# Optimization experiments

Hardware: AMD Instinct MI355X
Metric: run time of the kernel (lower is better)

The kernel has to match this reference:

```python
import jax, jax.numpy as jnp
import numpy as np
from jax import lax

B, D, BOND, OUT = 16384, 784, 5, 10

def setup_inputs() -> dict:
    key = jax.random.key(0)
    k = jax.random.split(key, 6)
    x = jax.random.uniform(k[0], (B, D), dtype=jnp.float32)
    core_first = jax.random.normal(k[1], (1, 2, BOND), dtype=jnp.float32) * 0.1
    cores_mid = jax.random.normal(k[2], (D - 2, BOND, 2, BOND), dtype=jnp.float32) * 0.1
    core_last = jax.random.normal(k[3], (BOND, 2, 1), dtype=jnp.float32) * 0.1
    # xavier_uniform for fc.weight with fan_in=1, fan_out=OUT
    bound = float(np.sqrt(6.0 / (1 + OUT)))
    fc_w = jax.random.uniform(k[4], (OUT, 1), dtype=jnp.float32, minval=-bound, maxval=bound)
    fc_b = jnp.zeros((OUT,), dtype=jnp.float32)
    return {"x": x, "core_first": core_first, "cores_mid": cores_mid,
            "core_last": core_last, "fc_w": fc_w, "fc_b": fc_b}

def reference(x, core_first, cores_mid, core_last, fc_w, fc_b):
    # x: [B, D] -> feature map [B, D, 2] = stack(1-x, x)
    xs = jnp.stack([1.0 - x, x], axis=-1)            # [B, D, 2]
    # first core: (1, 2, bond) -> initial carry [B, bond]
    carry0 = jnp.einsum('bi,ir->br', xs[:, 0], core_first[0])  # [B, bond]
    # sequential tensor-train contraction over middle sites via scan
    xs_mid = jnp.moveaxis(xs[:, 1:-1], 1, 0)          # [D-2, B, 2]
    def step(carry, inp):
        xi, core = inp                                # xi: [B,2], core: [bond,2,bond]
        carry = jnp.einsum('bl,bi,lir->br', carry, xi, core)
        return carry, None
    carry, _ = lax.scan(step, carry0, (xs_mid, cores_mid))
    # last core: (bond, 2, 1) -> scalar per batch element
    vlast = jnp.einsum('bi,li->bl', xs[:, -1], core_last[:, :, 0])  # [B, bond]
    res = jnp.sum(carry * vlast, axis=-1, keepdims=True)            # [B, 1]
    out = res @ fc_w.T + fc_b                          # [B, OUT]
    return out
```

## Files before the change

### kernel.cpp

```cpp
#include <hip/hip_runtime.h>


typedef float v4f __attribute__((ext_vector_type(4)));
typedef float v2f __attribute__((ext_vector_type(2)));

constexpr int Bn     = 16384;
constexpr int Dn     = 784;
constexpr int NOUT   = 10;
constexpr int NPAIR  = 390;
constexpr int PVEC   = 41;
constexpr int PMAT   = 22;
constexpr int RHP0   = 195;
constexpr int BWD_P0 = 349;
constexpr int PAIR_F = 100;
constexpr int PAIR_V = 25;

__device__ __forceinline__ v4f splat4(float x) { v4f v = {x, x, x, x}; return v; }
__device__ __forceinline__ v4f fma4(v4f a, v4f b, v4f c) {
    return __builtin_elementwise_fma(a, b, c);
}

struct Frag { v4f r[5]; float c4[5]; };
struct CMat { v4f row[5]; v4f c4v; float c44; };

__device__ __forceinline__ void build_C2(const float* s, v2f xA, v2f xB,
                                         CMat& CA, CMat& CB) {
    const float aA = xA[0], bA = xA[1], pA = aA * bA;
    const float aB = xB[0], bB = xB[1], pB = aB * bB;
    const v4f vaA = splat4(aA), vbA = splat4(bA), vpA = splat4(pA);
    const v4f vaB = splat4(aB), vbB = splat4(bB), vpB = splat4(pB);
    const v4f* s4 = (const v4f*)s;
#pragma unroll
    for (int l = 0; l < 5; ++l) {
        v4f q0 = s4[l], q1 = s4[5 + l], q2 = s4[10 + l], q3 = s4[15 + l];
        CA.row[l] = fma4(vpA, q3, fma4(vbA, q2, fma4(vaA, q1, q0)));
        CB.row[l] = fma4(vpB, q3, fma4(vbB, q2, fma4(vaB, q1, q0)));
    }
    {
        v4f q0 = s4[20], q1 = s4[21], q2 = s4[22], q3 = s4[23];
        CA.c4v = fma4(vpA, q3, fma4(vbA, q2, fma4(vaA, q1, q0)));
        CB.c4v = fma4(vpB, q3, fma4(vbB, q2, fma4(vaB, q1, q0)));
    }
    {
        v4f q = s4[24];
        CA.c44 = fmaf(pA, q[3], fmaf(bA, q[2], fmaf(aA, q[1], q[0])));
        CB.c44 = fmaf(pB, q[3], fmaf(bB, q[2], fmaf(aB, q[1], q[0])));
    }
}

__device__ __forceinline__ void matmul(const Frag& M, const CMat& C, Frag& T) {
#pragma unroll
    for (int i = 0; i < 5; ++i) {
        v4f acc  = splat4(M.r[i][0]) * C.row[0];
        float a4 = M.r[i][0] * C.c4v[0];
#pragma unroll
        for (int l = 1; l < 4; ++l) {
            acc = fma4(splat4(M.r[i][l]), C.row[l], acc);
            a4  = fmaf(M.r[i][l], C.c4v[l], a4);
        }
        acc = fma4(splat4(M.c4[i]), C.row[4], acc);
        a4  = fmaf(M.c4[i], C.c44, a4);
        T.r[i] = acc; T.c4[i] = a4;
    }
}

__device__ __forceinline__ void vecstep(v4f& cv, float& c4, const CMat& C) {
    v4f acc  = splat4(cv[0]) * C.row[0];
    float a4 = cv[0] * C.c4v[0];
#pragma unroll
    for (int l = 1; l < 4; ++l) {
        acc = fma4(splat4(cv[l]), C.row[l], acc);
        a4  = fmaf(cv[l], C.c4v[l], a4);
    }
    acc = fma4(splat4(c4), C.row[4], acc);
    a4  = fmaf(c4, C.c44, a4);
    cv = acc; c4 = a4;
}

__device__ __forceinline__ void sload(const v4f* src, v4f& a, v4f& b, int lane) {
    a = src[lane];
    if (lane < 36) b = src[64 + lane];
}
__device__ __forceinline__ void swrite(v4f* dst, v4f a, v4f b, int lane) {
    dst[lane] = a;
    if (lane < 36) dst[64 + lane] = b;
}

__global__ void prepack_pairs(const float* __restrict__ cm, float* __restrict__ pk)
{
    int idx = blockIdx.x * 256 + threadIdx.x;
    if (idx >= NPAIR * 100) return;
    int p = idx / 100, rest = idx - p * 100;
    int q = rest / 25, e = rest - q * 25;
    int l = e / 5, r = e - l * 5;
    int m1 = 2 * p + 1, m2 = 2 * p + 2;
    const float* L = cm + (size_t)(m1 * 5 + l) * 10;
    float acc = 0.f;
#pragma unroll
    for (int k = 0; k < 5; ++k) {
        float Lk = (q & 1) ? (L[5 + k] - L[k]) : L[k];
        const float* R = cm + (size_t)(m2 * 5 + k) * 10;
        float Rk = (q & 2) ? (R[5 + r] - R[r]) : R[r];
        acc = fmaf(Lk, Rk, acc);
    }
    int wl = l, wr = r;
    if (p >= BWD_P0) { wl = r; wr = l; }
    int off;
    if (wr < 4)      off = q * 20 + wl * 4 + wr;
    else if (wl < 4) off = 80 + q * 4 + wl;
    else             off = 96 + q;
    pk[(size_t)p * PAIR_F + off] = acc;
}

__global__ __launch_bounds__(512, 2)
void mps_half_kernel(const float* __restrict__ x,
                     const float* __restrict__ core_first,
                     const float* __restrict__ cores_mid,
                     const float* __restrict__ core_last,
                     const float* __restrict__ pk,
                     float* __restrict__ out)
{
    __shared__ v4f   pkbuf[8][2][100];
    __shared__ float matbuf[7][25][128];

    const int lane = threadIdx.x & 63;
    const int wave = threadIdx.x >> 6;
    const int g    = blockIdx.x >> 1;
    const int h    = blockIdx.x & 1;
    const int rowA = g * 128 + lane;
    const int rowB = rowA + 64;
    const v2f* __restrict__ xA2 = (const v2f*)(x + (size_t)rowA * Dn);
    const v2f* __restrict__ xB2 = (const v2f*)(x + (size_t)rowB * Dn);
    const v4f* __restrict__ pk4 = (const v4f*)pk;

    v4f* buf0 = &pkbuf[wave][0][0];
    v4f* buf1 = &pkbuf[wave][1][0];

    const bool isvec = (h == 0) ? (wave == 0) : (wave == 7);

    if (!isvec) {
        const int slot = (h == 0) ? (wave - 1) : wave;
        const int p0   = (h == 0) ? (PVEC + PMAT * (wave - 1))
                                  : (RHP0 + PMAT * wave);
        v4f sa, sb;
        sload(pk4 + (size_t)p0 * PAIR_V, sa, sb, lane);
        swrite(buf0, sa, sb, lane);
        sload(pk4 + (size_t)(p0 + 4) * PAIR_V, sa, sb, lane);
        v2f cA0 = xA2[p0 + 1], cA1 = xA2[p0 + 2], cA2 = xA2[p0 + 3], cA3 = xA2[p0 + 4];
        v2f cB0 = xB2[p0 + 1], cB1 = xB2[p0 + 2], cB2 = xB2[p0 + 3], cB3 = xB2[p0 + 4];

        Frag MA, TA, MB, TB;
        MA.r[0] = {1,0,0,0}; MA.r[1] = {0,1,0,0}; MA.r[2] = {0,0,1,0};
        MA.r[3] = {0,0,0,1}; MA.r[4] = {0,0,0,0};
        MA.c4[0] = 0; MA.c4[1] = 0; MA.c4[2] = 0; MA.c4[3] = 0; MA.c4[4] = 1;
        MB = MA;

#pragma unroll 1
        for (int c = 0; c < 6; ++c) {
            v4f* wb = (c & 1) ? buf0 : buf1;
            const float* rb = (const float*)((c & 1) ? buf1 : buf0);
            swrite(wb, sa, sb, lane);
            int ns = p0 + 4 * (c + 2);
            if (ns > NPAIR - 4) ns = NPAIR - 4;
            sload(pk4 + (size_t)ns * PAIR_V, sa, sb, lane);
            const int pn = p0 + 4 * (c + 1);
            v2f nA0 = xA2[pn + 1], nA1 = xA2[pn + 2], nA2 = xA2[pn + 3], nA3 = xA2[pn + 4];
            v2f nB0 = xB2[pn + 1], nB1 = xB2[pn + 2], nB2 = xB2[pn + 3], nB3 = xB2[pn + 4];
            CMat CA, CB;
            build_C2(rb + 0 * PAIR_F, cA0, cB0, CA, CB);
            matmul(MA, CA, TA); matmul(MB, CB, TB);
            build_C2(rb + 1 * PAIR_F, cA1, cB1, CA, CB);
            matmul(TA, CA, MA); matmul(TB, CB, MB);
            if (c < 5) {
                build_C2(rb + 2 * PAIR_F, cA2, cB2, CA, CB);
                matmul(MA, CA, TA); matmul(MB, CB, TB);
                build_C2(rb + 3 * PAIR_F, cA3, cB3, CA, CB);
                matmul(TA, CA, MA); matmul(TB, CB, MB);
            }
            cA0 = nA0; cA1 = nA1; cA2 = nA2; cA3 = nA3;
            cB0 = nB0; cB1 = nB1; cB2 = nB2; cB3 = nB3;
        }

#pragma unroll
        for (int i = 0; i < 5; ++i) {
#pragma unroll
            for (int r = 0; r < 4; ++r) {
                matbuf[slot][i * 5 + r][lane]      = MA.r[i][r];
                matbuf[slot][i * 5 + r][lane + 64] = MB.r[i][r];
            }
            matbuf[slot][i * 5 + 4][lane]      = MA.c4[i];
            matbuf[slot][i * 5 + 4][lane + 64] = MB.c4[i];
        }
        __syncthreads();
    } else if (h == 0) {
        v2f xA01 = xA2[0], xB01 = xB2[0];
        float clA[5], clB[5], cnA[5], cnB[5];
#pragma unroll
        for (int r = 0; r < 5; ++r) {
            float d = core_first[5 + r] - core_first[r];
            clA[r] = fmaf(xA01[0], d, core_first[r]);
            clB[r] = fmaf(xB01[0], d, core_first[r]);
        }
        const float* cm0 = cores_mid;
#pragma unroll
        for (int r = 0; r < 5; ++r) {
            float aA = 0.f, aB = 0.f;
#pragma unroll
            for (int l = 0; l < 5; ++l) {
                float base = cm0[l * 10 + r], d = cm0[l * 10 + 5 + r] - base;
                aA = fmaf(clA[l], fmaf(xA01[1], d, base), aA);
                aB = fmaf(clB[l], fmaf(xB01[1], d, base), aB);
            }
            cnA[r] = aA; cnB[r] = aB;
        }
        v4f cvA = {cnA[0], cnA[1], cnA[2], cnA[3]};
        v4f cvB = {cnB[0], cnB[1], cnB[2], cnB[3]};
        float c4A = cnA[4], c4B = cnB[4];

        v4f sa, sb;
        sload(pk4 + 0, sa, sb, lane);
        swrite(buf0, sa, sb, lane);
        sload(pk4 + (size_t)4 * PAIR_V, sa, sb, lane);
        v2f cA0 = xA2[1], cA1 = xA2[2], cA2 = xA2[3], cA3 = xA2[4];
        v2f cB0 = xB2[1], cB1 = xB2[2], cB2 = xB2[3], cB3 = xB2[4];

#pragma unroll 1
        for (int c = 0; c < 11; ++c) {
            v4f* wb = (c & 1) ? buf0 : buf1;
            const float* rb = (const float*)((c & 1) ? buf1 : buf0);
            swrite(wb, sa, sb, lane);
            int ns = 4 * (c + 2);
            if (ns > NPAIR - 4) ns = NPAIR - 4;
            sload(pk4 + (size_t)ns * PAIR_V, sa, sb, lane);
            const int pn = 4 * (c + 1);
            v2f nA0 = xA2[pn + 1], nA1 = xA2[pn + 2], nA2 = xA2[pn + 3], nA3 = xA2[pn + 4];
            v2f nB0 = xB2[pn + 1], nB1 = xB2[pn + 2], nB2 = xB2[pn + 3], nB3 = xB2[pn + 4];
            CMat CA, CB;
            build_C2(rb + 0 * PAIR_F, cA0, cB0, CA, CB);
            vecstep(cvA, c4A, CA); vecstep(cvB, c4B, CB);
            if (c < 10) {
                build_C2(rb + 1 * PAIR_F, cA1, cB1, CA, CB);
                vecstep(cvA, c4A, CA); vecstep(cvB, c4B, CB);
                build_C2(rb + 2 * PAIR_F, cA2, cB2, CA, CB);
                vecstep(cvA, c4A, CA); vecstep(cvB, c4B, CB);
                build_C2(rb + 3 * PAIR_F, cA3, cB3, CA, CB);
                vecstep(cvA, c4A, CA); vecstep(cvB, c4B, CB);
            }
            cA0 = nA0; cA1 = nA1; cA2 = nA2; cA3 = nA3;
            cB0 = nB0; cB1 = nB1; cB2 = nB2; cB3 = nB3;
        }
        clA[0] = cvA[0]; clA[1] = cvA[1]; clA[2] = cvA[2]; clA[3] = cvA[3]; clA[4] = c4A;
        clB[0] = cvB[0]; clB[1] = cvB[1]; clB[2] = cvB[2]; clB[3] = cvB[3]; clB[4] = c4B;

        __syncthreads();
#pragma unroll 1
        for (int w2 = 0; w2 < 7; ++w2) {
            float vA[5], vB[5];
#pragma unroll
            for (int r = 0; r < 5; ++r) {
                vA[r] = clA[0] * matbuf[w2][r][lane];
                vB[r] = clB[0] * matbuf[w2][r][lane + 64];
            }
#pragma unroll
            for (int l = 1; l < 5; ++l)
#pragma unroll
                for (int r = 0; r < 5; ++r) {
                    vA[r] = fmaf(clA[l], matbuf[w2][l * 5 + r][lane],      vA[r]);
                    vB[r] = fmaf(clB[l], matbuf[w2][l * 5 + r][lane + 64], vB[r]);
                }
#pragma unroll
            for (int r = 0; r < 5; ++r) { clA[r] = vA[r]; clB[r] = vB[r]; }
        }
        float* oA = out + (size_t)rowA * NOUT;
        float* oB = out + (size_t)rowB * NOUT;
#pragma unroll
        for (int i = 0; i < 5; ++i) { oA[i] = clA[i]; oB[i] = clB[i]; }
    } else {
        v2f xAz = xA2[391], xBz = xB2[391];
        float vlA[5], vlB[5], vnA[5], vnB[5];
#pragma unroll
        for (int l = 0; l < 5; ++l) {
            float base = core_last[2 * l], d = core_last[2 * l + 1] - base;
            vlA[l] = fmaf(xAz[1], d, base);
            vlB[l] = fmaf(xBz[1], d, base);
        }
        const float* cmL = cores_mid + (size_t)781 * 50;
#pragma unroll
        for (int l = 0; l < 5; ++l) {
            float aA = 0.f, aB = 0.f;
#pragma unroll
            for (int r = 0; r < 5; ++r) {
                float base = cmL[l * 10 + r], d = cmL[l * 10 + 5 + r] - base;
                aA = fmaf(fmaf(xAz[0], d, base), vlA[r], aA);
                aB = fmaf(fmaf(xBz[0], d, base), vlB[r], aB);
            }
            vnA[l] = aA; vnB[l] = aB;
        }
        v4f cvA = {vnA[0], vnA[1], vnA[2], vnA[3]};
        v4f cvB = {vnB[0], vnB[1], vnB[2], vnB[3]};
        float c4A = vnA[4], c4B = vnB[4];

        v4f sa, sb;
        sload(pk4 + (size_t)386 * PAIR_V, sa, sb, lane);
        swrite(buf0, sa, sb, lane);
        sload(pk4 + (size_t)382 * PAIR_V, sa, sb, lane);
        v2f cA0 = xA2[390], cA1 = xA2[389], cA2 = xA2[388], cA3 = xA2[387];
        v2f cB0 = xB2[390], cB1 = xB2[389], cB2 = xB2[388], cB3 = xB2[387];

#pragma unroll 1
        for (int c = 0; c < 11; ++c) {
            v4f* wb = (c & 1) ? buf0 : buf1;
            const float* rb = (const float*)((c & 1) ? buf1 : buf0);
            swrite(wb, sa, sb, lane);
            int ns = 386 - 4 * (c + 2);
            sload(pk4 + (size_t)ns * PAIR_V, sa, sb, lane);
            const int bn = 386 - 4 * (c + 1);
            v2f nA0 = xA2[bn + 4], nA1 = xA2[bn + 3], nA2 = xA2[bn + 2], nA3 = xA2[bn + 1];
            v2f nB0 = xB2[bn + 4], nB1 = xB2[bn + 3], nB2 = xB2[bn + 2], nB3 = xB2[bn + 1];
            CMat CA, CB;
            build_C2(rb + 3 * PAIR_F, cA0, cB0, CA, CB);
            vecstep(cvA, c4A, CA); vecstep(cvB, c4B, CB);
            if (c < 10) {
                build_C2(rb + 2 * PAIR_F, cA1, cB1, CA, CB);
                vecstep(cvA, c4A, CA); vecstep(cvB, c4B, CB);
                build_C2(rb + 1 * PAIR_F, cA2, cB2, CA, CB);
                vecstep(cvA, c4A, CA); vecstep(cvB, c4B, CB);
                build_C2(rb + 0 * PAIR_F, cA3, cB3, CA, CB);
                vecstep(cvA, c4A, CA); vecstep(cvB, c4B, CB);
            }
            cA0 = nA0; cA1 = nA1; cA2 = nA2; cA3 = nA3;
            cB0 = nB0; cB1 = nB1; cB2 = nB2; cB3 = nB3;
        }
        float uA[5] = {cvA[0], cvA[1], cvA[2], cvA[3], c4A};
        float uB[5] = {cvB[0], cvB[1], cvB[2], cvB[3], c4B};

        __syncthreads();
#pragma unroll 1
        for (int w2 = 6; w2 >= 0; --w2) {
            float vA[5], vB[5];
#pragma unroll
            for (int i = 0; i < 5; ++i) {
                float aA = matbuf[w2][i * 5][lane]      * uA[0];
                float aB = matbuf[w2][i * 5][lane + 64] * uB[0];
#pragma unroll
                for (int l = 1; l < 5; ++l) {
                    aA = fmaf(matbuf[w2][i * 5 + l][lane],      uA[l], aA);
                    aB = fmaf(matbuf[w2][i * 5 + l][lane + 64], uB[l], aB);
                }
                vA[i] = aA; vB[i] = aB;
            }
#pragma unroll
            for (int i = 0; i < 5; ++i) { uA[i] = vA[i]; uB[i] = vB[i]; }
        }
        float* oA = out + (size_t)rowA * NOUT;
        float* oB = out + (size_t)rowB * NOUT;
#pragma unroll
        for (int i = 0; i < 5; ++i) { oA[5 + i] = uA[i]; oB[5 + i] = uB[i]; }
    }
}

__global__ __launch_bounds__(256)
void finish_out(const float* __restrict__ fc_w, const float* __restrict__ fc_b,
                float* __restrict__ out)
{
    int row = blockIdx.x * 256 + threadIdx.x;
    float* o = out + (size_t)row * NOUT;
    v2f e0 = *(const v2f*)(o + 0);
    v2f e1 = *(const v2f*)(o + 2);
    v2f e2 = *(const v2f*)(o + 4);
    v2f e3 = *(const v2f*)(o + 6);
    v2f e4 = *(const v2f*)(o + 8);
    float res = e0[0] * e2[1];
    res = fmaf(e0[1], e3[0], res);
    res = fmaf(e1[0], e3[1], res);
    res = fmaf(e1[1], e4[0], res);
    res = fmaf(e2[0], e4[1], res);
#pragma unroll
    for (int j = 0; j < NOUT; ++j) o[j] = fmaf(res, fc_w[j], fc_b[j]);
}

extern "C" void kernel_launch(void* const* d_in, const int* in_sizes, int n_in,
                              void* d_out, int out_size, void* d_ws, size_t ws_size,
                              hipStream_t stream) {
    const float* x          = (const float*)d_in[0];
    const float* core_first = (const float*)d_in[1];
    const float* cores_mid  = (const float*)d_in[2];
    const float* core_last  = (const float*)d_in[3];
    const float* fc_w       = (const float*)d_in[4];
    const float* fc_b       = (const float*)d_in[5];
    float* out              = (float*)d_out;
    float* pk               = (float*)d_ws;

    hipLaunchKernelGGL(prepack_pairs, dim3((NPAIR * 100 + 255) / 256), dim3(256),
                       0, stream, cores_mid, pk);
    hipLaunchKernelGGL(mps_half_kernel, dim3(256), dim3(512), 0, stream,
                       x, core_first, cores_mid, core_last, pk, out);
    hipLaunchKernelGGL(finish_out, dim3(Bn / 256), dim3(256), 0, stream,
                       fc_w, fc_b, out);
}
```

Before: 148.6 us.

## Split the chain across 12 waves with a two-phase matrix handoff

Each block now runs 12 waves instead of 8. The vector-carry waves handle fewer pairs (two per chunk instead of four), and eleven matrix waves each compute a 16-pair product. Matrix results go to shared memory in two phases separated by barriers, which lets 6 slots be reused for 11 products. The final dot product moves into its own kernel that reads a packed left/right layout from the output buffer. The aim is more parallelism along the sequential chain, paid for with extra barriers, an extra launch and a larger block that may hurt occupancy.

```diff
diff --git a/kernel.cpp b/kernel.cpp
--- a/kernel.cpp
+++ b/kernel.cpp
@@ -8,12 +8,14 @@
 constexpr int Dn     = 784;
 constexpr int NOUT   = 10;
 constexpr int NPAIR  = 390;
-constexpr int PVEC   = 41;
-constexpr int PMAT   = 22;
+constexpr int PVEC   = 19;
+constexpr int NMAT   = 11;
+constexpr int PMAT   = 16;
 constexpr int RHP0   = 195;
-constexpr int BWD_P0 = 349;
+constexpr int BWD_P0 = 371;
 constexpr int PAIR_F = 100;
 constexpr int PAIR_V = 25;
+constexpr int WROFF  = Bn * 5;
 
 __device__ __forceinline__ v4f splat4(float x) { v4f v = {x, x, x, x}; return v; }
 __device__ __forceinline__ v4f fma4(v4f a, v4f b, v4f c) {
@@ -48,7 +50,7 @@
     }
 }
 
-__device__ __forceinline__ void matmul(const Frag& M, const CMat& C, Frag& T) {
+__device__ __forceinline__ void matstep(Frag& M, const CMat& C) {
 #pragma unroll
     for (int i = 0; i < 5; ++i) {
         v4f acc  = splat4(M.r[i][0]) * C.row[0];
@@ -60,7 +62,7 @@
         }
         acc = fma4(splat4(M.c4[i]), C.row[4], acc);
         a4  = fmaf(M.c4[i], C.c44, a4);
-        T.r[i] = acc; T.c4[i] = a4;
+        M.r[i] = acc; M.c4[i] = a4;
     }
 }
 
@@ -84,6 +86,12 @@
 __device__ __forceinline__ void swrite(v4f* dst, v4f a, v4f b, int lane) {
     dst[lane] = a;
     if (lane < 36) dst[64 + lane] = b;
+}
+__device__ __forceinline__ void sload50(const v4f* src, v4f& a, int lane) {
+    if (lane < 50) a = src[lane];
+}
+__device__ __forceinline__ void swrite50(v4f* dst, v4f a, int lane) {
+    if (lane < 50) dst[lane] = a;
 }
 
 __global__ void prepack_pairs(const float* __restrict__ cm, float* __restrict__ pk)
@@ -112,7 +120,7 @@
     pk[(size_t)p * PAIR_F + off] = acc;
 }
 
-__global__ __launch_bounds__(512, 2)
+__global__ __launch_bounds__(768, 3)
 void mps_half_kernel(const float* __restrict__ x,
                      const float* __restrict__ core_first,
                      const float* __restrict__ cores_mid,
@@ -120,8 +128,8 @@
                      const float* __restrict__ pk,
                      float* __restrict__ out)
 {
-    __shared__ v4f   pkbuf[8][2][100];
-    __shared__ float matbuf[7][25][128];
+    __shared__ v4f   pkbuf[12][2][100];
+    __shared__ float matbuf[6][25][128];
 
     const int lane = threadIdx.x & 63;
     const int wave = threadIdx.x >> 6;
@@ -136,12 +144,9 @@
     v4f* buf0 = &pkbuf[wave][0][0];
     v4f* buf1 = &pkbuf[wave][1][0];
 
-    const bool isvec = (h == 0) ? (wave == 0) : (wave == 7);
-
-    if (!isvec) {
-        const int slot = (h == 0) ? (wave - 1) : wave;
-        const int p0   = (h == 0) ? (PVEC + PMAT * (wave - 1))
-                                  : (RHP0 + PMAT * wave);
+    if (wave != 0) {
+        const int s  = wave - 1;
+        const int p0 = (h == 0 ? PVEC : RHP0) + PMAT * s;
         v4f sa, sb;
         sload(pk4 + (size_t)p0 * PAIR_V, sa, sb, lane);
         swrite(buf0, sa, sb, lane);
@@ -149,14 +154,14 @@
         v2f cA0 = xA2[p0 + 1], cA1 = xA2[p0 + 2], cA2 = xA2[p0 + 3], cA3 = xA2[p0 + 4];
         v2f cB0 = xB2[p0 + 1], cB1 = xB2[p0 + 2], cB2 = xB2[p0 + 3], cB3 = xB2[p0 + 4];
 
-        Frag MA, TA, MB, TB;
+        Frag MA, MB;
         MA.r[0] = {1,0,0,0}; MA.r[1] = {0,1,0,0}; MA.r[2] = {0,0,1,0};
         MA.r[3] = {0,0,0,1}; MA.r[4] = {0,0,0,0};
         MA.c4[0] = 0; MA.c4[1] = 0; MA.c4[2] = 0; MA.c4[3] = 0; MA.c4[4] = 1;
         MB = MA;
 
 #pragma unroll 1
-        for (int c = 0; c < 6; ++c) {
+        for (int c = 0; c < 4; ++c) {
             v4f* wb = (c & 1) ? buf0 : buf1;
             const float* rb = (const float*)((c & 1) ? buf1 : buf0);
             swrite(wb, sa, sb, lane);
@@ -168,28 +173,45 @@
             v2f nB0 = xB2[pn + 1], nB1 = xB2[pn + 2], nB2 = xB2[pn + 3], nB3 = xB2[pn + 4];
             CMat CA, CB;
             build_C2(rb + 0 * PAIR_F, cA0, cB0, CA, CB);
-            matmul(MA, CA, TA); matmul(MB, CB, TB);
+            matstep(MA, CA); matstep(MB, CB);
             build_C2(rb + 1 * PAIR_F, cA1, cB1, CA, CB);
-            matmul(TA, CA, MA); matmul(TB, CB, MB);
-            if (c < 5) {
-                build_C2(rb + 2 * PAIR_F, cA2, cB2, CA, CB);
-                matmul(MA, CA, TA); matmul(MB, CB, TB);
-                build_C2(rb + 3 * PAIR_F, cA3, cB3, CA, CB);
-                matmul(TA, CA, MA); matmul(TB, CB, MB);
-            }
+            matstep(MA, CA); matstep(MB, CB);
+            build_C2(rb + 2 * PAIR_F, cA2, cB2, CA, CB);
+            matstep(MA, CA); matstep(MB, CB);
+            build_C2(rb + 3 * PAIR_F, cA3, cB3, CA, CB);
+            matstep(MA, CA); matstep(MB, CB);
             cA0 = nA0; cA1 = nA1; cA2 = nA2; cA3 = nA3;
             cB0 = nB0; cB1 = nB1; cB2 = nB2; cB3 = nB3;
         }
 
-#pragma unroll
-        for (int i = 0; i < 5; ++i) {
-#pragma unroll
-            for (int r = 0; r < 4; ++r) {
-                matbuf[slot][i * 5 + r][lane]      = MA.r[i][r];
-                matbuf[slot][i * 5 + r][lane + 64] = MB.r[i][r];
-            }
-            matbuf[slot][i * 5 + 4][lane]      = MA.c4[i];
-            matbuf[slot][i * 5 + 4][lane + 64] = MB.c4[i];
+        const bool ph1 = (h == 0) ? (s < 6) : (s >= 5);
+        const int  k   = ph1 ? ((h == 0) ? s : 10 - s)
+                             : ((h == 0) ? s - 6 : 4 - s);
+        if (ph1) {
+#pragma unroll
+            for (int i = 0; i < 5; ++i) {
+#pragma unroll
+                for (int r = 0; r < 4; ++r) {
+                    matbuf[k][i * 5 + r][lane]      = MA.r[i][r];
+                    matbuf[k][i * 5 + r][lane + 64] = MB.r[i][r];
+                }
+                matbuf[k][i * 5 + 4][lane]      = MA.c4[i];
+                matbuf[k][i * 5 + 4][lane + 64] = MB.c4[i];
+            }
+        }
+        __syncthreads();
+        __syncthreads();
+        if (!ph1) {
+#pragma unroll
+            for (int i = 0; i < 5; ++i) {
+#pragma unroll
+                for (int r = 0; r < 4; ++r) {
+                    matbuf[k][i * 5 + r][lane]      = MA.r[i][r];
+                    matbuf[k][i * 5 + r][lane + 64] = MB.r[i][r];
+                }
+                matbuf[k][i * 5 + 4][lane]      = MA.c4[i];
+                matbuf[k][i * 5 + 4][lane + 64] = MB.c4[i];
+            }
         }
         __syncthreads();
     } else if (h == 0) {
@@ -217,62 +239,76 @@
         v4f cvB = {cnB[0], cnB[1], cnB[2], cnB[3]};
         float c4A = cnA[4], c4B = cnB[4];
 
-        v4f sa, sb;
-        sload(pk4 + 0, sa, sb, lane);
-        swrite(buf0, sa, sb, lane);
-        sload(pk4 + (size_t)4 * PAIR_V, sa, sb, lane);
-        v2f cA0 = xA2[1], cA1 = xA2[2], cA2 = xA2[3], cA3 = xA2[4];
-        v2f cB0 = xB2[1], cB1 = xB2[2], cB2 = xB2[3], cB3 = xB2[4];
-
-#pragma unroll 1
-        for (int c = 0; c < 11; ++c) {
+        v4f sa;
+        sload50(pk4 + 0, sa, lane);
+        swrite50(buf0, sa, lane);
+        sload50(pk4 + (size_t)2 * PAIR_V, sa, lane);
+        v2f cA0 = xA2[1], cA1 = xA2[2];
+        v2f cB0 = xB2[1], cB1 = xB2[2];
+
+#pragma unroll 1
+        for (int c = 0; c < 10; ++c) {
             v4f* wb = (c & 1) ? buf0 : buf1;
             const float* rb = (const float*)((c & 1) ? buf1 : buf0);
-            swrite(wb, sa, sb, lane);
-            int ns = 4 * (c + 2);
-            if (ns > NPAIR - 4) ns = NPAIR - 4;
-            sload(pk4 + (size_t)ns * PAIR_V, sa, sb, lane);
-            const int pn = 4 * (c + 1);
-            v2f nA0 = xA2[pn + 1], nA1 = xA2[pn + 2], nA2 = xA2[pn + 3], nA3 = xA2[pn + 4];
-            v2f nB0 = xB2[pn + 1], nB1 = xB2[pn + 2], nB2 = xB2[pn + 3], nB3 = xB2[pn + 4];
+            swrite50(wb, sa, lane);
+            int ns = 2 * (c + 2);
+            sload50(pk4 + (size_t)ns * PAIR_V, sa, lane);
+            const int pn = 2 * (c + 1);
+            v2f nA0 = xA2[pn + 1], nA1 = xA2[pn + 2];
+            v2f nB0 = xB2[pn + 1], nB1 = xB2[pn + 2];
             CMat CA, CB;
             build_C2(rb + 0 * PAIR_F, cA0, cB0, CA, CB);
             vecstep(cvA, c4A, CA); vecstep(cvB, c4B, CB);
-            if (c < 10) {
+            if (c < 9) {
                 build_C2(rb + 1 * PAIR_F, cA1, cB1, CA, CB);
                 vecstep(cvA, c4A, CA); vecstep(cvB, c4B, CB);
-                build_C2(rb + 2 * PAIR_F, cA2, cB2, CA, CB);
-                vecstep(cvA, c4A, CA); vecstep(cvB, c4B, CB);
-                build_C2(rb + 3 * PAIR_F, cA3, cB3, CA, CB);
-                vecstep(cvA, c4A, CA); vecstep(cvB, c4B, CB);
-            }
-            cA0 = nA0; cA1 = nA1; cA2 = nA2; cA3 = nA3;
-            cB0 = nB0; cB1 = nB1; cB2 = nB2; cB3 = nB3;
+            }
+            cA0 = nA0; cA1 = nA1; cB0 = nB0; cB1 = nB1;
         }
         clA[0] = cvA[0]; clA[1] = cvA[1]; clA[2] = cvA[2]; clA[3] = cvA[3]; clA[4] = c4A;
         clB[0] = cvB[0]; clB[1] = cvB[1]; clB[2] = cvB[2]; clB[3] = cvB[3]; clB[4] = c4B;
 
         __syncthreads();
 #pragma unroll 1
-        for (int w2 = 0; w2 < 7; ++w2) {
+        for (int k = 0; k < 6; ++k) {
             float vA[5], vB[5];
 #pragma unroll
             for (int r = 0; r < 5; ++r) {
-                vA[r] = clA[0] * matbuf[w2][r][lane];
-                vB[r] = clB[0] * matbuf[w2][r][lane + 64];
+                vA[r] = clA[0] * matbuf[k][r][lane];
+                vB[r] = clB[0] * matbuf[k][r][lane + 64];
             }
 #pragma unroll
             for (int l = 1; l < 5; ++l)
 #pragma unroll
                 for (int r = 0; r < 5; ++r) {
-                    vA[r] = fmaf(clA[l], matbuf[w2][l * 5 + r][lane],      vA[r]);
-                    vB[r] = fmaf(clB[l], matbuf[w2][l * 5 + r][lane + 64], vB[r]);
+                    vA[r] = fmaf(clA[l], matbuf[k][l * 5 + r][lane],      vA[r]);
+                    vB[r] = fmaf(clB[l], matbuf[k][l * 5 + r][lane + 64], vB[r]);
                 }
 #pragma unroll
             for (int r = 0; r < 5; ++r) { clA[r] = vA[r]; clB[r] = vB[r]; }
         }
-        float* oA = out + (size_t)rowA * NOUT;
-        float* oB = out + (size_t)rowB * NOUT;
+        __syncthreads();
+        __syncthreads();
+#pragma unroll 1
+        for (int k = 0; k < 5; ++k) {
+            float vA[5], vB[5];
+#pragma unroll
+            for (int r = 0; r < 5; ++r) {
+                vA[r] = clA[0] * matbuf[k][r][lane];
+                vB[r] = clB[0] * matbuf[k][r][lane + 64];
+            }
+#pragma unroll
+            for (int l = 1; l < 5; ++l)
+#pragma unroll
+                for (int r = 0; r < 5; ++r) {
+                    vA[r] = fmaf(clA[l], matbuf[k][l * 5 + r][lane],      vA[r]);
+                    vB[r] = fmaf(clB[l], matbuf[k][l * 5 + r][lane + 64], vB[r]);
+                }
+#pragma unroll
+            for (int r = 0; r < 5; ++r) { clA[r] = vA[r]; clB[r] = vB[r]; }
+        }
+        float* oA = out + (size_t)rowA * 5;
+        float* oB = out + (size_t)rowB * 5;
 #pragma unroll
         for (int i = 0; i < 5; ++i) { oA[i] = clA[i]; oB[i] = clB[i]; }
     } else {
@@ -300,83 +336,100 @@
         v4f cvB = {vnB[0], vnB[1], vnB[2], vnB[3]};
         float c4A = vnA[4], c4B = vnB[4];
 
-        v4f sa, sb;
-        sload(pk4 + (size_t)386 * PAIR_V, sa, sb, lane);
-        swrite(buf0, sa, sb, lane);
-        sload(pk4 + (size_t)382 * PAIR_V, sa, sb, lane);
-        v2f cA0 = xA2[390], cA1 = xA2[389], cA2 = xA2[388], cA3 = xA2[387];
-        v2f cB0 = xB2[390], cB1 = xB2[389], cB2 = xB2[388], cB3 = xB2[387];
-
-#pragma unroll 1
-        for (int c = 0; c < 11; ++c) {
+        v4f sa;
+        sload50(pk4 + (size_t)388 * PAIR_V, sa, lane);
+        swrite50(buf0, sa, lane);
+        sload50(pk4 + (size_t)386 * PAIR_V, sa, lane);
+        v2f cA0 = xA2[390], cA1 = xA2[389];
+        v2f cB0 = xB2[390], cB1 = xB2[389];
+
+#pragma unroll 1
+        for (int c = 0; c < 10; ++c) {
             v4f* wb = (c & 1) ? buf0 : buf1;
             const float* rb = (const float*)((c & 1) ? buf1 : buf0);
-            swrite(wb, sa, sb, lane);
-            int ns = 386 - 4 * (c + 2);
-            sload(pk4 + (size_t)ns * PAIR_V, sa, sb, lane);
-            const int bn = 386 - 4 * (c + 1);
-            v2f nA0 = xA2[bn + 4], nA1 = xA2[bn + 3], nA2 = xA2[bn + 2], nA3 = xA2[bn + 1];
-            v2f nB0 = xB2[bn + 4], nB1 = xB2[bn + 3], nB2 = xB2[bn + 2], nB3 = xB2[bn + 1];
+            swrite50(wb, sa, lane);
+            int ns = 388 - 2 * (c + 2);
+            sload50(pk4 + (size_t)ns * PAIR_V, sa, lane);
+            const int bn = 388 - 2 * (c + 1);
+            v2f nA0 = xA2[bn + 2], nA1 = xA2[bn + 1];
+            v2f nB0 = xB2[bn + 2], nB1 = xB2[bn + 1];
             CMat CA, CB;
-            build_C2(rb + 3 * PAIR_F, cA0, cB0, CA, CB);
+            build_C2(rb + 1 * PAIR_F, cA0, cB0, CA, CB);
             vecstep(cvA, c4A, CA); vecstep(cvB, c4B, CB);
-            if (c < 10) {
-                build_C2(rb + 2 * PAIR_F, cA1, cB1, CA, CB);
+            if (c < 9) {
+                build_C2(rb + 0 * PAIR_F, cA1, cB1, CA, CB);
                 vecstep(cvA, c4A, CA); vecstep(cvB, c4B, CB);
-                build_C2(rb + 1 * PAIR_F, cA2, cB2, CA, CB);
-                vecstep(cvA, c4A, CA); vecstep(cvB, c4B, CB);
-                build_C2(rb + 0 * PAIR_F, cA3, cB3, CA, CB);
-                vecstep(cvA, c4A, CA); vecstep(cvB, c4B, CB);
-            }
-            cA0 = nA0; cA1 = nA1; cA2 = nA2; cA3 = nA3;
-            cB0 = nB0; cB1 = nB1; cB2 = nB2; cB3 = nB3;
+            }
+            cA0 = nA0; cA1 = nA1; cB0 = nB0; cB1 = nB1;
         }
         float uA[5] = {cvA[0], cvA[1], cvA[2], cvA[3], c4A};
         float uB[5] = {cvB[0], cvB[1], cvB[2], cvB[3], c4B};
 
         __syncthreads();
 #pragma unroll 1
-        for (int w2 = 6; w2 >= 0; --w2) {
+        for (int k = 0; k < 6; ++k) {
             float vA[5], vB[5];
 #pragma unroll
             for (int i = 0; i < 5; ++i) {
-                float aA = matbuf[w2][i * 5][lane]      * uA[0];
-                float aB = matbuf[w2][i * 5][lane + 64] * uB[0];
+                float aA = matbuf[k][i * 5][lane]      * uA[0];
+                float aB = matbuf[k][i * 5][lane + 64] * uB[0];
 #pragma unroll
                 for (int l = 1; l < 5; ++l) {
-                    aA = fmaf(matbuf[w2][i * 5 + l][lane],      uA[l], aA);
-                    aB = fmaf(matbuf[w2][i * 5 + l][lane + 64], uB[l], aB);
+                    aA = fmaf(matbuf[k][i * 5 + l][lane],      uA[l], aA);
+                    aB = fmaf(matbuf[k][i * 5 + l][lane + 64], uB[l], aB);
                 }
                 vA[i] = aA; vB[i] = aB;
             }
 #pragma unroll
             for (int i = 0; i < 5; ++i) { uA[i] = vA[i]; uB[i] = vB[i]; }
         }
-        float* oA = out + (size_t)rowA * NOUT;
-        float* oB = out + (size_t)rowB * NOUT;
-#pragma unroll
-        for (int i = 0; i < 5; ++i) { oA[5 + i] = uA[i]; oB[5 + i] = uB[i]; }
+        __syncthreads();
+        __syncthreads();
+#pragma unroll 1
+        for (int k = 0; k < 5; ++k) {
+            float vA[5], vB[5];
+#pragma unroll
+            for (int i = 0; i < 5; ++i) {
+                float aA = matbuf[k][i * 5][lane]      * uA[0];
+                float aB = matbuf[k][i * 5][lane + 64] * uB[0];
+#pragma unroll
+                for (int l = 1; l < 5; ++l) {
+                    aA = fmaf(matbuf[k][i * 5 + l][lane],      uA[l], aA);
+                    aB = fmaf(matbuf[k][i * 5 + l][lane + 64], uB[l], aB);
+                }
+                vA[i] = aA; vB[i] = aB;
+            }
+#pragma unroll
+            for (int i = 0; i < 5; ++i) { uA[i] = vA[i]; uB[i] = vB[i]; }
+        }
+        float* oA = out + WROFF + (size_t)rowA * 5;
+        float* oB = out + WROFF + (size_t)rowB * 5;
+#pragma unroll
+        for (int i = 0; i < 5; ++i) { oA[i] = uA[i]; oB[i] = uB[i]; }
     }
 }
 
 __global__ __launch_bounds__(256)
-void finish_out(const float* __restrict__ fc_w, const float* __restrict__ fc_b,
-                float* __restrict__ out)
+void finish_dot(const float* __restrict__ outF, float* __restrict__ res)
 {
-    int row = blockIdx.x * 256 + threadIdx.x;
-    float* o = out + (size_t)row * NOUT;
-    v2f e0 = *(const v2f*)(o + 0);
-    v2f e1 = *(const v2f*)(o + 2);
-    v2f e2 = *(const v2f*)(o + 4);
-    v2f e3 = *(const v2f*)(o + 6);
-    v2f e4 = *(const v2f*)(o + 8);
-    float res = e0[0] * e2[1];
-    res = fmaf(e0[1], e3[0], res);
-    res = fmaf(e1[0], e3[1], res);
-    res = fmaf(e1[1], e4[0], res);
-    res = fmaf(e2[0], e4[1], res);
-#pragma unroll
-    for (int j = 0; j < NOUT; ++j) o[j] = fmaf(res, fc_w[j], fc_b[j]);
+    int r = blockIdx.x * 256 + threadIdx.x;
+    const float* vl = outF + (size_t)r * 5;
+    const float* wr = outF + WROFF + (size_t)r * 5;
+    float s = vl[0] * wr[0];
+#pragma unroll
+    for (int i = 1; i < 5; ++i) s = fmaf(vl[i], wr[i], s);
+    res[r] = s;
+}
+
+__global__ __launch_bounds__(256)
+void finish_out(const float* __restrict__ res, const float* __restrict__ fc_w,
+                const float* __restrict__ fc_b, float* __restrict__ out)
+{
+    int r = blockIdx.x * 256 + threadIdx.x;
+    float rv = res[r];
+    float* o = out + (size_t)r * NOUT;
+#pragma unroll
+    for (int j = 0; j < NOUT; ++j) o[j] = fmaf(rv, fc_w[j], fc_b[j]);
 }
 
 extern "C" void kernel_launch(void* const* d_in, const int* in_sizes, int n_in,
@@ -390,11 +443,14 @@
     const float* fc_b       = (const float*)d_in[5];
     float* out              = (float*)d_out;
     float* pk               = (float*)d_ws;
+    float* res              = (float*)d_ws;
 
     hipLaunchKernelGGL(prepack_pairs, dim3((NPAIR * 100 + 255) / 256), dim3(256),
                        0, stream, cores_mid, pk);
-    hipLaunchKernelGGL(mps_half_kernel, dim3(256), dim3(512), 0, stream,
+    hipLaunchKernelGGL(mps_half_kernel, dim3(256), dim3(768), 0, stream,
                        x, core_first, cores_mid, core_last, pk, out);
+    hipLaunchKernelGGL(finish_dot, dim3(Bn / 256), dim3(256), 0, stream,
+                       out, res);
     hipLaunchKernelGGL(finish_out, dim3(Bn / 256), dim3(256), 0, stream,
-                       fc_w, fc_b, out);
-}
+                       res, fc_w, fc_b, out);
+}
```

Result: slower. 521.3 us (+250.8%).
